# Optimization experiments

Measured on AMD Instinct MI355X. Metric: run time of the kernel, lower is better.

## Reference

```python
import jax, jax.numpy as jnp
import numpy as np

B, M, N = 256, 256, 256

def setup_inputs() -> dict:
    key = jax.random.key(0)
    k1, k2 = jax.random.split(key)
    x_real = jax.random.normal(k1, (B, M, N), dtype=jnp.float32)
    x_imag = jax.random.normal(k2, (B, M, N), dtype=jnp.float32)
    return {"x_real": x_real, "x_imag": x_imag}

def reference(x_real, x_imag):
    # complex k-space input; original used complex128 via numpy on host,
    # we use complex64 (the natural accelerator precision), same math.
    x = jax.lax.complex(x_real, x_imag)  # [B, M, N]
    axes = (-2, -1)
    # centered 2D IFFT per sample (ifft_along_dim): fftshift(ifft2(ifftshift(x)))
    y = jnp.fft.fftshift(jnp.fft.ifft2(jnp.fft.ifftshift(x, axes=axes), axes=axes), axes=axes)
    y = y.reshape(-1, 1, M, N)  # (-1, 1, M, N) as in call()
    return (jnp.real(y), jnp.imag(y))
```

## Files before the change

### kernel.cpp

```cpp
#include <hip/hip_runtime.h>

namespace {

constexpr int NN   = 256;
constexpr int BMN  = 256 * 256 * 256;
constexpr int LPAD = 272;

struct cpx { float re, im; };

__device__ __forceinline__ cpx cadd(cpx a, cpx b){ return cpx{a.re + b.re, a.im + b.im}; }
__device__ __forceinline__ cpx csub(cpx a, cpx b){ return cpx{a.re - b.re, a.im - b.im}; }
__device__ __forceinline__ cpx cmul(cpx a, cpx b){ return cpx{a.re*b.re - a.im*b.im, a.re*b.im + a.im*b.re}; }
__device__ __forceinline__ cpx cmuli(cpx a){ return cpx{-a.im, a.re}; }

__device__ __forceinline__ void r4(cpx a, cpx b, cpx c, cpx d,
                                   cpx& y0, cpx& y1, cpx& y2, cpx& y3) {
  cpx apc = cadd(a, c), amc = csub(a, c);
  cpx bpd = cadd(b, d), bmd = csub(b, d);
  cpx ib  = cmuli(bmd);
  y0 = cadd(apc, bpd);
  y1 = cadd(amc, ib);
  y2 = csub(apc, bpd);
  y3 = csub(amc, ib);
}

__device__ __forceinline__ void ifft16(cpx x[16]) {
  constexpr float WC[10] = { 1.f,  0.9238795325112867f,  0.7071067811865476f,  0.3826834323650898f, 0.f,
                            -0.3826834323650898f, -0.7071067811865476f, -0.9238795325112867f, -1.f,
                            -0.9238795325112867f };
  constexpr float WS[10] = { 0.f,  0.3826834323650898f,  0.7071067811865476f,  0.9238795325112867f, 1.f,
                             0.9238795325112867f,  0.7071067811865476f,  0.3826834323650898f,  0.f,
                            -0.3826834323650898f };
  cpx B[4][4];
#pragma unroll
  for (int n1 = 0; n1 < 4; ++n1)
    r4(x[n1], x[n1 + 4], x[n1 + 8], x[n1 + 12],
       B[n1][0], B[n1][1], B[n1][2], B[n1][3]);
#pragma unroll
  for (int n1 = 1; n1 < 4; ++n1)
#pragma unroll
    for (int k2 = 1; k2 < 4; ++k2)
      B[n1][k2] = cmul(B[n1][k2], cpx{WC[n1 * k2], WS[n1 * k2]});
#pragma unroll
  for (int k2 = 0; k2 < 4; ++k2)
    r4(B[0][k2], B[1][k2], B[2][k2], B[3][k2],
       x[k2], x[k2 + 4], x[k2 + 8], x[k2 + 12]);
}

__device__ __forceinline__ void twiddle256(cpx a[16], int t) {
  const float base = 0.024543692606170259f * (float)t;
#pragma unroll
  for (int k1 = 1; k1 < 16; ++k1) {
    float s, c;
    __sincosf(base * (float)k1, &s, &c);
    a[k1] = cmul(a[k1], cpx{c, s});
  }
}

__global__ __launch_bounds__(256)
void k_ifft_rows(const float* __restrict__ xr, const float* __restrict__ xi,
                 float* __restrict__ yr, float* __restrict__ yi) {
  __shared__ float Lr[16 * LPAD];
  __shared__ float Li[16 * LPAD];
  const int tid = threadIdx.x;
  const int t   = tid & 15;
  const int ll  = tid >> 4;

  const size_t blk = (size_t)blockIdx.x * (16 * NN);
  const float4* sr4 = reinterpret_cast<const float4*>(xr + blk);
  const float4* si4 = reinterpret_cast<const float4*>(xi + blk);

#pragma unroll
  for (int q = 0; q < 4; ++q) {
    const int fi   = (q << 8) + tid;
    const int line = fi >> 6;
    const int slot = fi & 63;
    *reinterpret_cast<float4*>(&Lr[line * LPAD + slot * 4]) = sr4[fi];
    *reinterpret_cast<float4*>(&Li[line * LPAD + slot * 4]) = si4[fi];
  }
  __syncthreads();

  cpx a[16];
  {
    const float* lr = Lr + ll * LPAD;
    const float* li = Li + ll * LPAD;
#pragma unroll
    for (int j = 0; j < 16; ++j) {
      const int idx = (((j << 4) | t) ^ 128);
      a[j] = cpx{ lr[idx], li[idx] };
    }
  }
  ifft16(a);
  twiddle256(a, t);
  __syncthreads();

  {
    float* lr = Lr + ll * LPAD;
    float* li = Li + ll * LPAD;
#pragma unroll
    for (int k1 = 0; k1 < 16; ++k1) { lr[k1 * 17 + t] = a[k1].re; li[k1 * 17 + t] = a[k1].im; }
    __syncthreads();
#pragma unroll
    for (int n2 = 0; n2 < 16; ++n2) { a[n2].re = lr[t * 17 + n2]; a[n2].im = li[t * 17 + n2]; }
  }
  ifft16(a);
  __syncthreads();

  {
    float* lr = Lr + ll * LPAD;
    float* li = Li + ll * LPAD;
#pragma unroll
    for (int k = 0; k < 16; ++k) {
      const int idx = (((k << 4) | t) ^ 128);
      lr[idx] = a[k].re;
      li[idx] = a[k].im;
    }
  }
  __syncthreads();

  float4* dr4 = reinterpret_cast<float4*>(yr + blk);
  float4* di4 = reinterpret_cast<float4*>(yi + blk);
#pragma unroll
  for (int q = 0; q < 4; ++q) {
    const int fi   = (q << 8) + tid;
    const int line = fi >> 6;
    const int slot = fi & 63;
    dr4[fi] = *reinterpret_cast<const float4*>(&Lr[line * LPAD + slot * 4]);
    di4[fi] = *reinterpret_cast<const float4*>(&Li[line * LPAD + slot * 4]);
  }
}

__global__ __launch_bounds__(512)
void k_ifft_cols(float* __restrict__ yr, float* __restrict__ yi) {
  __shared__ float lbuf[32 * 273];
  const int tid = threadIdx.x;
  const int c   = tid & 31;
  const int t   = tid >> 5;
  const int b   = blockIdx.x >> 3;
  const int c0  = (blockIdx.x & 7) << 5;
  const int base = b * 65536 + c0 + c;

  cpx a[16];
#pragma unroll
  for (int j = 0; j < 16; ++j) {
    const int m = (((j << 4) | t) ^ 128);
    a[j] = cpx{ yr[base + m * NN], yi[base + m * NN] };
  }
  ifft16(a);
  twiddle256(a, t);

  {
    float* L = lbuf + c * 273;
#pragma unroll
    for (int k1 = 0; k1 < 16; ++k1) L[k1 * 17 + t] = a[k1].re;
    __syncthreads();
    float br[16];
#pragma unroll
    for (int n2 = 0; n2 < 16; ++n2) br[n2] = L[t * 17 + n2];
    __syncthreads();
#pragma unroll
    for (int k1 = 0; k1 < 16; ++k1) L[k1 * 17 + t] = a[k1].im;
    __syncthreads();
#pragma unroll
    for (int n2 = 0; n2 < 16; ++n2) { a[n2].im = L[t * 17 + n2]; a[n2].re = br[n2]; }
  }

  ifft16(a);
  constexpr float sc = 1.0f / 65536.0f;
#pragma unroll
  for (int k = 0; k < 16; ++k) {
    const int m = (((k << 4) | t) ^ 128);
    yr[base + m * NN] = a[k].re * sc;
    yi[base + m * NN] = a[k].im * sc;
  }
}

}

extern "C" void kernel_launch(void* const* d_in, const int* in_sizes, int n_in,
                              void* d_out, int out_size, void* d_ws, size_t ws_size,
                              hipStream_t stream) {
  const float* xr = (const float*)d_in[0];
  const float* xi = (const float*)d_in[1];
  float* yr = (float*)d_out;
  float* yi = yr + BMN;

  k_ifft_rows<<<4096, 256, 0, stream>>>(xr, xi, yr, yi);
  k_ifft_cols<<<2048, 512, 0, stream>>>(yr, yi);
}
```

Before: 86.54 us.

## Fuse row and column IFFT passes per image with fp16 intermediate workspace

After: 81.70 us. 1.06x faster.

```diff
diff --git a/kernel.cpp b/kernel.cpp
--- a/kernel.cpp
+++ b/kernel.cpp
@@ -1,10 +1,13 @@
 #include <hip/hip_runtime.h>
+#include <hip/hip_fp16.h>
 
 namespace {
 
 constexpr int NN   = 256;
 constexpr int BMN  = 256 * 256 * 256;
 constexpr int LPAD = 272;
+
+typedef float f4 __attribute__((ext_vector_type(4)));
 
 struct cpx { float re, im; };
 
@@ -57,121 +60,137 @@
   }
 }
 
-__global__ __launch_bounds__(256)
-void k_ifft_rows(const float* __restrict__ xr, const float* __restrict__ xi,
-                 float* __restrict__ yr, float* __restrict__ yi) {
-  __shared__ float Lr[16 * LPAD];
-  __shared__ float Li[16 * LPAD];
-  const int tid = threadIdx.x;
-  const int t   = tid & 15;
-  const int ll  = tid >> 4;
-
-  const size_t blk = (size_t)blockIdx.x * (16 * NN);
-  const float4* sr4 = reinterpret_cast<const float4*>(xr + blk);
-  const float4* si4 = reinterpret_cast<const float4*>(xi + blk);
-
-#pragma unroll
-  for (int q = 0; q < 4; ++q) {
-    const int fi   = (q << 8) + tid;
-    const int line = fi >> 6;
-    const int slot = fi & 63;
-    *reinterpret_cast<float4*>(&Lr[line * LPAD + slot * 4]) = sr4[fi];
-    *reinterpret_cast<float4*>(&Li[line * LPAD + slot * 4]) = si4[fi];
-  }
-  __syncthreads();
-
-  cpx a[16];
+__global__ __launch_bounds__(1024)
+void k_ifft2d(const float* __restrict__ xr, const float* __restrict__ xi,
+              __half* __restrict__ wr, __half* __restrict__ wi,
+              float* __restrict__ yr, float* __restrict__ yi) {
+  __shared__ float SM[2 * 64 * LPAD];
+  float* Lr = SM;
+  float* Li = SM + 64 * LPAD;
+
+  const int tid  = threadIdx.x;
+  const size_t ibase = (size_t)blockIdx.x * (NN * NN);
+
   {
-    const float* lr = Lr + ll * LPAD;
-    const float* li = Li + ll * LPAD;
-#pragma unroll
-    for (int j = 0; j < 16; ++j) {
-      const int idx = (((j << 4) | t) ^ 128);
-      a[j] = cpx{ lr[idx], li[idx] };
+    const int t  = tid & 15;
+    const int ll = tid >> 4;
+    for (int it = 0; it < 4; ++it) {
+      const size_t off = ibase + (size_t)it * (64 * NN);
+      const f4* sr4 = reinterpret_cast<const f4*>(xr + off);
+      const f4* si4 = reinterpret_cast<const f4*>(xi + off);
+#pragma unroll
+      for (int q = 0; q < 4; ++q) {
+        const int fi   = (q << 10) + tid;
+        const int line = fi >> 6;
+        const int slot = fi & 63;
+        *reinterpret_cast<f4*>(&Lr[line * LPAD + slot * 4]) = sr4[fi];
+        *reinterpret_cast<f4*>(&Li[line * LPAD + slot * 4]) = si4[fi];
+      }
+      __syncthreads();
+
+      cpx a[16];
+      {
+        const float* lr = Lr + ll * LPAD;
+        const float* li = Li + ll * LPAD;
+#pragma unroll
+        for (int j = 0; j < 16; ++j) {
+          const int idx = (((j << 4) | t) ^ 128);
+          a[j] = cpx{ lr[idx], li[idx] };
+        }
+      }
+      ifft16(a);
+      twiddle256(a, t);
+      __syncthreads();
+
+      {
+        float* lr = Lr + ll * LPAD;
+        float* li = Li + ll * LPAD;
+#pragma unroll
+        for (int k1 = 0; k1 < 16; ++k1) { lr[k1 * 17 + t] = a[k1].re; li[k1 * 17 + t] = a[k1].im; }
+        __syncthreads();
+#pragma unroll
+        for (int n2 = 0; n2 < 16; ++n2) { a[n2].re = lr[t * 17 + n2]; a[n2].im = li[t * 17 + n2]; }
+      }
+      ifft16(a);
+      __syncthreads();
+
+      {
+        float* lr = Lr + ll * LPAD;
+        float* li = Li + ll * LPAD;
+#pragma unroll
+        for (int k = 0; k < 16; ++k) {
+          const int idx = (((k << 4) | t) ^ 128);
+          lr[idx] = a[k].re;
+          li[idx] = a[k].im;
+        }
+      }
+      __syncthreads();
+
+      constexpr float s1 = 1.0f / 256.0f;
+      uint2* dr = reinterpret_cast<uint2*>(wr + off);
+      uint2* di = reinterpret_cast<uint2*>(wi + off);
+#pragma unroll
+      for (int q = 0; q < 4; ++q) {
+        const int fi   = (q << 10) + tid;
+        const int p    = fi << 2;
+        const int line = p >> 8;
+        const int idx  = p & 255;
+        const f4 vr = *reinterpret_cast<const f4*>(&Lr[line * LPAD + idx]);
+        const f4 vi = *reinterpret_cast<const f4*>(&Li[line * LPAD + idx]);
+        union { __half2 h[2]; uint2 u; } hr, hi;
+        hr.h[0] = __floats2half2_rn(vr.x * s1, vr.y * s1);
+        hr.h[1] = __floats2half2_rn(vr.z * s1, vr.w * s1);
+        hi.h[0] = __floats2half2_rn(vi.x * s1, vi.y * s1);
+        hi.h[1] = __floats2half2_rn(vi.z * s1, vi.w * s1);
+        dr[fi] = hr.u;
+        di[fi] = hi.u;
+      }
+      __syncthreads();
     }
   }
-  ifft16(a);
-  twiddle256(a, t);
-  __syncthreads();
 
   {
-    float* lr = Lr + ll * LPAD;
-    float* li = Li + ll * LPAD;
-#pragma unroll
-    for (int k1 = 0; k1 < 16; ++k1) { lr[k1 * 17 + t] = a[k1].re; li[k1 * 17 + t] = a[k1].im; }
-    __syncthreads();
-#pragma unroll
-    for (int n2 = 0; n2 < 16; ++n2) { a[n2].re = lr[t * 17 + n2]; a[n2].im = li[t * 17 + n2]; }
-  }
-  ifft16(a);
-  __syncthreads();
-
-  {
-    float* lr = Lr + ll * LPAD;
-    float* li = Li + ll * LPAD;
-#pragma unroll
-    for (int k = 0; k < 16; ++k) {
-      const int idx = (((k << 4) | t) ^ 128);
-      lr[idx] = a[k].re;
-      li[idx] = a[k].im;
+    const int c  = tid & 63;
+    const int tg = tid >> 6;
+    float* TR = SM;
+    for (int ct = 0; ct < 4; ++ct) {
+      __syncthreads();
+      const size_t base = ibase + (ct << 6) + c;
+
+      cpx a[16];
+#pragma unroll
+      for (int j = 0; j < 16; ++j) {
+        const int m = (((j << 4) | tg) ^ 128);
+        a[j] = cpx{ __half2float(wr[base + m * NN]), __half2float(wi[base + m * NN]) };
+      }
+      ifft16(a);
+      twiddle256(a, tg);
+
+      {
+        float* L = TR + c * 273;
+#pragma unroll
+        for (int k1 = 0; k1 < 16; ++k1) L[k1 * 17 + tg] = a[k1].re;
+        __syncthreads();
+        float br[16];
+#pragma unroll
+        for (int n2 = 0; n2 < 16; ++n2) br[n2] = L[tg * 17 + n2];
+        __syncthreads();
+#pragma unroll
+        for (int k1 = 0; k1 < 16; ++k1) L[k1 * 17 + tg] = a[k1].im;
+        __syncthreads();
+#pragma unroll
+        for (int n2 = 0; n2 < 16; ++n2) { a[n2].im = L[tg * 17 + n2]; a[n2].re = br[n2]; }
+      }
+
+      ifft16(a);
+      constexpr float s2 = 1.0f / 256.0f;
+#pragma unroll
+      for (int k = 0; k < 16; ++k) {
+        const int m = (((k << 4) | tg) ^ 128);
+        __builtin_nontemporal_store(a[k].re * s2, &yr[base + m * NN]);
+        __builtin_nontemporal_store(a[k].im * s2, &yi[base + m * NN]);
+      }
     }
-  }
-  __syncthreads();
-
-  float4* dr4 = reinterpret_cast<float4*>(yr + blk);
-  float4* di4 = reinterpret_cast<float4*>(yi + blk);
-#pragma unroll
-  for (int q = 0; q < 4; ++q) {
-    const int fi   = (q << 8) + tid;
-    const int line = fi >> 6;
-    const int slot = fi & 63;
-    dr4[fi] = *reinterpret_cast<const float4*>(&Lr[line * LPAD + slot * 4]);
-    di4[fi] = *reinterpret_cast<const float4*>(&Li[line * LPAD + slot * 4]);
-  }
-}
-
-__global__ __launch_bounds__(512)
-void k_ifft_cols(float* __restrict__ yr, float* __restrict__ yi) {
-  __shared__ float lbuf[32 * 273];
-  const int tid = threadIdx.x;
-  const int c   = tid & 31;
-  const int t   = tid >> 5;
-  const int b   = blockIdx.x >> 3;
-  const int c0  = (blockIdx.x & 7) << 5;
-  const int base = b * 65536 + c0 + c;
-
-  cpx a[16];
-#pragma unroll
-  for (int j = 0; j < 16; ++j) {
-    const int m = (((j << 4) | t) ^ 128);
-    a[j] = cpx{ yr[base + m * NN], yi[base + m * NN] };
-  }
-  ifft16(a);
-  twiddle256(a, t);
-
-  {
-    float* L = lbuf + c * 273;
-#pragma unroll
-    for (int k1 = 0; k1 < 16; ++k1) L[k1 * 17 + t] = a[k1].re;
-    __syncthreads();
-    float br[16];
-#pragma unroll
-    for (int n2 = 0; n2 < 16; ++n2) br[n2] = L[t * 17 + n2];
-    __syncthreads();
-#pragma unroll
-    for (int k1 = 0; k1 < 16; ++k1) L[k1 * 17 + t] = a[k1].im;
-    __syncthreads();
-#pragma unroll
-    for (int n2 = 0; n2 < 16; ++n2) { a[n2].im = L[t * 17 + n2]; a[n2].re = br[n2]; }
-  }
-
-  ifft16(a);
-  constexpr float sc = 1.0f / 65536.0f;
-#pragma unroll
-  for (int k = 0; k < 16; ++k) {
-    const int m = (((k << 4) | t) ^ 128);
-    yr[base + m * NN] = a[k].re * sc;
-    yi[base + m * NN] = a[k].im * sc;
   }
 }
 
@@ -184,7 +203,8 @@
   const float* xi = (const float*)d_in[1];
   float* yr = (float*)d_out;
   float* yi = yr + BMN;
-
-  k_ifft_rows<<<4096, 256, 0, stream>>>(xr, xi, yr, yi);
-  k_ifft_cols<<<2048, 512, 0, stream>>>(yr, yi);
-}
+  __half* wr = (__half*)d_ws;
+  __half* wi = wr + BMN;
+
+  k_ifft2d<<<256, 1024, 0, stream>>>(xr, xi, wr, wi, yr, yi);
+}
```
